# Kernel optimization log

Hardware: AMD Instinct MI355X
Metric: run time of the kernel (lower is better)

## Reference

```python
import jax, jax.numpy as jnp
import numpy as np

N, E, IN_DIM, D, T, L, B, SLEN, C = 50000, 600000, 128, 128, 4, 2, 2048, 16, 16


def _deg_inv_sqrt(idx, n, dtype):
    deg = jax.ops.segment_sum(jnp.ones(idx.shape, dtype=dtype), idx, num_segments=n)
    return jnp.where(deg > 0, deg ** -0.5, 0.0).astype(dtype)


def gcn_conv(h, edge_index, W, b):
    # PyG GCNConv: add self loops, symmetric norm, x@W, scatter-add, +bias
    n = h.shape[0]
    loop = jnp.arange(n)
    row = jnp.concatenate([edge_index[0], loop])
    col = jnp.concatenate([edge_index[1], loop])
    dis = _deg_inv_sqrt(col, n, h.dtype)
    norm = dis[row] * dis[col]              # [E+N]
    xw = h @ W                               # [N, D]
    msgs = xw[row] * norm[:, None]           # [E+N, D] gather
    out = jax.ops.segment_sum(msgs, col, num_segments=n)
    return out + b


def re_conv(r, edge_index, node_type, W, wtype, b):
    # REConv(norm='both'): left-norm by src out-degree, x@W, type weight,
    # scatter-add to dst, right-norm by dst in-degree, +bias, relu
    n = r.shape[0]
    row, col = edge_index
    dl = _deg_inv_sqrt(row, n, r.dtype)
    x = (r * dl[:, None]) @ W                # [N, T]
    x = x * wtype[node_type][:, None]
    out = jax.ops.segment_sum(x[row], col, num_segments=n)
    dr = _deg_inv_sqrt(col, n, r.dtype)
    out = out * dr[:, None] + b
    return jax.nn.relu(out)


def setup_inputs() -> dict:
    key = jax.random.key(0)
    ks = jax.random.split(key, 10)
    x = jax.random.normal(ks[0], (N, IN_DIM), dtype=jnp.float32)
    label = jax.random.randint(ks[1], (N,), 0, C)
    seqs = jax.random.randint(ks[2], (B, SLEN), 0, N)
    edge_index = jax.random.randint(ks[3], (2, E), 0, N)
    node_type = jnp.sort(jax.random.randint(ks[4], (N,), 0, T))
    s_in = 1.0 / np.sqrt(IN_DIM)
    s_d = 1.0 / np.sqrt(D)
    fcW = jax.random.normal(ks[5], (T, IN_DIM, D), dtype=jnp.float32) * s_in
    fcB = jnp.zeros((T, D), dtype=jnp.float32)
    gcnW = jax.random.normal(ks[6], (L, D, D), dtype=jnp.float32) * s_d
    gcnB = jnp.zeros((L, D), dtype=jnp.float32)
    reW = jax.random.normal(ks[7], (L, T, T), dtype=jnp.float32) * 0.5
    re_wtype = jnp.ones((L, T), dtype=jnp.float32)
    reB = jnp.zeros((L, T), dtype=jnp.float32)
    predW = jax.random.normal(ks[8], (D, C), dtype=jnp.float32) * s_d
    predB = jnp.zeros((C,), dtype=jnp.float32)
    return {"x": x, "label": label, "seqs": seqs, "edge_index": edge_index,
            "node_type": node_type, "fcW": fcW, "fcB": fcB, "gcnW": gcnW,
            "gcnB": gcnB, "reW": reW, "re_wtype": re_wtype, "reB": reB,
            "predW": predW, "predB": predB}


def reference(x, label, seqs, edge_index, node_type, fcW, fcB, gcnW, gcnB,
              reW, re_wtype, reB, predW, predB):
    n = x.shape[0]
    # per-type input projection; node_type is sorted so this equals
    # torch.cat([fc[t](x[node_type==t]) for t])
    h_all = jnp.einsum('ni,tio->tno', x, fcW) + fcB[:, None, :]  # [T, N, D]
    gh = h_all[node_type, jnp.arange(n)]                          # [N, D]
    r = jnp.eye(fcW.shape[0], dtype=x.dtype)[node_type]           # [N, T]
    for l in range(gcnW.shape[0]):
        gh = jax.nn.relu(gcn_conv(gh, edge_index, gcnW[l], gcnB[l]))
        r = re_conv(r, edge_index, node_type, reW[l], re_wtype[l], reB[l])
    ego = seqs[:, 0]
    output = gh[ego] @ predW + predB                               # [B, C]
    return output, label[ego]
```

## Files before the change

### kernel.cpp

```cpp
#include <hip/hip_runtime.h>
#include <hip/hip_bf16.h>


typedef __attribute__((ext_vector_type(8))) short short8;
typedef __attribute__((ext_vector_type(4))) float f32x4;
typedef unsigned short u16;

__device__ __forceinline__ float bf2f(u16 u) {
  union { float f; unsigned int i; } v; v.i = (unsigned int)u << 16; return v.f;
}
__device__ __forceinline__ u16 f2bf(float f) {
  union { float f; unsigned int i; } v; v.f = f;
  return (u16)((v.i + 0x7FFF + ((v.i >> 16) & 1)) >> 16);
}

#define NPB 64

__global__ void k_wt(const float* __restrict__ fcW, const float* __restrict__ gcnW,
                     u16* __restrict__ wt, int T, int total) {
  int i = blockIdx.x * 256 + threadIdx.x;
  if (i >= total) return;
  int m = i >> 14;
  int dk = i & 16383;
  int d = dk >> 7, k = dk & 127;
  const float* src = (m < T) ? (fcW + ((size_t)m << 14)) : (gcnW + ((size_t)(m - T) << 14));
  wt[i] = f2bf(src[k * 128 + d]);
}

#define SWZ(row, byte) ((byte) ^ (((row) & 15) << 4))

__device__ __forceinline__ void stage_wt(char* smem_wt, const u16* __restrict__ wtg,
                                         int t) {
  int row = t >> 1;
  int h = (t & 1) * 64;
  const u16* src = wtg + row * 128 + h;
#pragma unroll
  for (int j = 0; j < 8; ++j) {
    short8 v = *(const short8*)(src + j * 8);
    int byte = row * 256 + (h + j * 8) * 2;
    *(short8*)(smem_wt + SWZ(row, byte)) = v;
  }
}

__device__ __forceinline__ void mfma_core(const char* smem_xs, const char* smem_wt,
                                          int t, f32x4 acc[4][2]) {
  const int lane = t & 63, w = t >> 6;
  const int lr = lane & 15, lk = lane >> 4;
#pragma unroll
  for (int ks = 0; ks < 4; ++ks) {
    const int kb = ks * 64 + lk * 16;
    short8 a[4], b[2];
#pragma unroll
    for (int rg = 0; rg < 4; ++rg) {
      int row = rg * 16 + lr;
      a[rg] = *(const short8*)(smem_xs + SWZ(row, row * 256 + kb));
    }
#pragma unroll
    for (int ch = 0; ch < 2; ++ch) {
      int row = w * 32 + ch * 16 + lr;
      b[ch] = *(const short8*)(smem_wt + SWZ(row, row * 256 + kb));
    }
#pragma unroll
    for (int rg = 0; rg < 4; ++rg)
#pragma unroll
      for (int ch = 0; ch < 2; ++ch)
        acc[rg][ch] = __builtin_amdgcn_mfma_f32_16x16x32_bf16(a[rg], b[ch], acc[rg][ch], 0, 0, 0);
  }
}

__global__ __launch_bounds__(256) void k_fc(const float* __restrict__ x,
                                            const int* __restrict__ node_type,
                                            const u16* __restrict__ wt_fc,
                                            const float* __restrict__ fcB,
                                            u16* __restrict__ gh, int n_nodes) {
  __shared__ char smem[49152];
  char* smem_xs = smem;
  char* smem_wt = smem + 16384;
  const int t = threadIdx.x;
  const int nbase = blockIdx.x * NPB;
  const int nend = min(nbase + NPB, n_nodes);
  const int t0 = node_type[nbase];
  const int t1 = node_type[nend - 1];

  {
    int row = t >> 2;
    int c0 = (t & 3) * 32;
    int node = nbase + row;
    float xv[32];
    if (node < n_nodes) {
      const float4* src = (const float4*)(x + (size_t)node * 128 + c0);
#pragma unroll
      for (int j = 0; j < 8; ++j) ((float4*)xv)[j] = src[j];
    } else {
#pragma unroll
      for (int j = 0; j < 32; ++j) xv[j] = 0.0f;
    }
#pragma unroll
    for (int j = 0; j < 4; ++j) {
      u16 tmp[8];
#pragma unroll
      for (int q = 0; q < 8; ++q) tmp[q] = f2bf(xv[j * 8 + q]);
      int byte = row * 256 + (c0 + j * 8) * 2;
      *(short8*)(smem_xs + SWZ(row, byte)) = *(short8*)tmp;
    }
  }

  const int lane = t & 63, w = t >> 6;
  const int lr = lane & 15, lk = lane >> 4;

  for (int tt = t0; tt <= t1; ++tt) {
    if (tt > t0) __syncthreads();
    stage_wt(smem_wt, wt_fc + ((size_t)tt << 14), t);
    __syncthreads();

    f32x4 acc[4][2];
#pragma unroll
    for (int rg = 0; rg < 4; ++rg)
#pragma unroll
      for (int ch = 0; ch < 2; ++ch) acc[rg][ch] = (f32x4){0.f, 0.f, 0.f, 0.f};
    mfma_core(smem_xs, smem_wt, t, acc);

#pragma unroll
    for (int rg = 0; rg < 4; ++rg) {
#pragma unroll
      for (int reg = 0; reg < 4; ++reg) {
        int node = nbase + rg * 16 + lk * 4 + reg;
        if (node < n_nodes && node_type[node] == tt) {
#pragma unroll
          for (int ch = 0; ch < 2; ++ch) {
            int dout = w * 32 + ch * 16 + lr;
            gh[(size_t)node * 128 + dout] = f2bf(acc[rg][ch][reg] + fcB[tt * 128 + dout]);
          }
        }
      }
    }
  }
}

__global__ __launch_bounds__(256) void k_gemm_scale(const u16* __restrict__ ghin,
                                                    const u16* __restrict__ wtg,
                                                    const float* __restrict__ dis,
                                                    u16* __restrict__ xws, int n_nodes) {
  __shared__ char smem[49152];
  char* smem_xs = smem;
  char* smem_wt = smem + 16384;
  const int t = threadIdx.x;
  const int nbase = blockIdx.x * NPB;

  {
    int row = t >> 2;
    int c0 = (t & 3) * 32;
    int node = nbase + row;
    if (node < n_nodes) {
      const u16* src = ghin + (size_t)node * 128 + c0;
#pragma unroll
      for (int j = 0; j < 4; ++j) {
        short8 v = *(const short8*)(src + j * 8);
        int byte = row * 256 + (c0 + j * 8) * 2;
        *(short8*)(smem_xs + SWZ(row, byte)) = v;
      }
    } else {
      short8 z = (short8){0, 0, 0, 0, 0, 0, 0, 0};
#pragma unroll
      for (int j = 0; j < 4; ++j) {
        int byte = row * 256 + (c0 + j * 8) * 2;
        *(short8*)(smem_xs + SWZ(row, byte)) = z;
      }
    }
  }
  stage_wt(smem_wt, wtg, t);
  __syncthreads();

  f32x4 acc[4][2];
#pragma unroll
  for (int rg = 0; rg < 4; ++rg)
#pragma unroll
    for (int ch = 0; ch < 2; ++ch) acc[rg][ch] = (f32x4){0.f, 0.f, 0.f, 0.f};
  mfma_core(smem_xs, smem_wt, t, acc);

  const int lane = t & 63, w = t >> 6;
  const int lr = lane & 15, lk = lane >> 4;
#pragma unroll
  for (int rg = 0; rg < 4; ++rg) {
#pragma unroll
    for (int reg = 0; reg < 4; ++reg) {
      int node = nbase + rg * 16 + lk * 4 + reg;
      if (node < n_nodes) {
        float s = dis[node];
#pragma unroll
        for (int ch = 0; ch < 2; ++ch) {
          int dout = w * 32 + ch * 16 + lr;
          xws[(size_t)node * 128 + dout] = f2bf(acc[rg][ch][reg] * s);
        }
      }
    }
  }
}

__global__ void k_zero(int* __restrict__ p, int n) {
  int i = blockIdx.x * 256 + threadIdx.x;
  if (i < n) p[i] = 0;
}

__global__ void k_count(const int* __restrict__ col, int* __restrict__ ecnt, int e) {
  int i = blockIdx.x * 256 + threadIdx.x;
  if (i < e) atomicAdd(&ecnt[col[i]], 1);
}

__global__ __launch_bounds__(256) void k_scan1(const int* __restrict__ ecnt,
                                               int* __restrict__ scanex,
                                               int* __restrict__ partials, int n) {
  __shared__ int s[256];
  const int t = threadIdx.x;
  const int i = blockIdx.x * 256 + t;
  int v = (i < n) ? ecnt[i] : 0;
  s[t] = v;
  __syncthreads();
  for (int off = 1; off < 256; off <<= 1) {
    int add = (t >= off) ? s[t - off] : 0;
    __syncthreads();
    s[t] += add;
    __syncthreads();
  }
  if (i < n) scanex[i] = s[t] - v;
  if (t == 255) partials[blockIdx.x] = s[t];
}

__global__ __launch_bounds__(256) void k_scan2(int* __restrict__ partials, int np) {
  __shared__ int s[256];
  const int t = threadIdx.x;
  int v = (t < np) ? partials[t] : 0;
  s[t] = v;
  __syncthreads();
  for (int off = 1; off < 256; off <<= 1) {
    int add = (t >= off) ? s[t - off] : 0;
    __syncthreads();
    s[t] += add;
    __syncthreads();
  }
  if (t < np) partials[t] = s[t] - v;
}

__global__ void k_scan3(const int* __restrict__ scanex, const int* __restrict__ partials,
                        const int* __restrict__ ecnt, int* __restrict__ col_ptr,
                        int* __restrict__ cursor, float* __restrict__ dis,
                        int n, int e_total) {
  int i = blockIdx.x * 256 + threadIdx.x;
  if (i < n) {
    int p = scanex[i] + partials[i >> 8];
    col_ptr[i] = p;
    cursor[i] = p;
    dis[i] = rsqrtf((float)(ecnt[i] + 1));
  }
  if (i == 0) col_ptr[n] = e_total;
}

__global__ void k_fill(const int* __restrict__ row, const int* __restrict__ col,
                       int* __restrict__ cursor, int* __restrict__ edge_row, int e) {
  int i = blockIdx.x * 256 + threadIdx.x;
  if (i < e) {
    int c = col[i];
    int pos = atomicAdd(&cursor[c], 1);
    edge_row[pos] = row[i];
  }
}

__global__ __launch_bounds__(256) void k_gather(const int* __restrict__ col_ptr,
                                                const int* __restrict__ edge_row,
                                                const u16* __restrict__ xws,
                                                const float* __restrict__ dis,
                                                const float* __restrict__ bias,
                                                u16* __restrict__ gh, int n_nodes) {
  const int t = threadIdx.x;
  const int node = blockIdx.x * 4 + (t >> 6);
  if (node >= n_nodes) return;
  const int lane = t & 63;
  const int g = lane & 15;
  const int s = lane >> 4;
  float acc[8] = {0.f, 0.f, 0.f, 0.f, 0.f, 0.f, 0.f, 0.f};
  if (s == 0) {
    short8 v = *(const short8*)(xws + (size_t)node * 128 + g * 8);
#pragma unroll
    for (int j = 0; j < 8; ++j) acc[j] = bf2f((u16)v[j]);
  }
  const int e0 = col_ptr[node], e1 = col_ptr[node + 1];
  for (int e = e0 + s; e < e1; e += 4) {
    int r = edge_row[e];
    short8 v = *(const short8*)(xws + (size_t)r * 128 + g * 8);
#pragma unroll
    for (int j = 0; j < 8; ++j) acc[j] += bf2f((u16)v[j]);
  }
#pragma unroll
  for (int j = 0; j < 8; ++j) {
    acc[j] += __shfl_xor(acc[j], 16);
    acc[j] += __shfl_xor(acc[j], 32);
  }
  if (s == 0) {
    float ds = dis[node];
    u16 o[8];
#pragma unroll
    for (int j = 0; j < 8; ++j)
      o[j] = f2bf(fmaxf(acc[j] * ds + bias[g * 8 + j], 0.f));
    *(short8*)(gh + (size_t)node * 128 + g * 8) = *(short8*)o;
  }
}

__global__ void k_pred(const u16* __restrict__ gh, const int* __restrict__ seqs,
                       const int* __restrict__ label, const float* __restrict__ predW,
                       const float* __restrict__ predB, float* __restrict__ out,
                       float* __restrict__ out_label, int b_total, int n_classes,
                       int slen) {
  int tid = blockIdx.x * 256 + threadIdx.x;
  int b = tid / n_classes;
  if (b >= b_total) return;
  int c = tid - b * n_classes;
  int ego = seqs[(size_t)b * slen];
  const u16* g = gh + (size_t)ego * 128;
  float s = predB[c];
#pragma unroll 8
  for (int i = 0; i < 128; ++i) s += bf2f(g[i]) * predW[i * n_classes + c];
  out[(size_t)b * n_classes + c] = s;
  if (c == 0) out_label[b] = (float)label[ego];
}

extern "C" void kernel_launch(void* const* d_in, const int* in_sizes, int n_in,
                              void* d_out, int out_size, void* d_ws, size_t ws_size,
                              hipStream_t stream) {
  const float* x     = (const float*)d_in[0];
  const int*   label = (const int*)d_in[1];
  const int*   seqs  = (const int*)d_in[2];
  const int*   edge  = (const int*)d_in[3];
  const int*   ntype = (const int*)d_in[4];
  const float* fcW   = (const float*)d_in[5];
  const float* fcB   = (const float*)d_in[6];
  const float* gcnW  = (const float*)d_in[7];
  const float* gcnB  = (const float*)d_in[8];
  const float* predW = (const float*)d_in[12];
  const float* predB = (const float*)d_in[13];

  const int n = in_sizes[0] / 128;
  const int e = in_sizes[3] / 2;
  const int T = in_sizes[5] / (128 * 128);
  const int L = in_sizes[8] / 128;
  const int C = in_sizes[13];
  const int slen = 16;
  const int b_total = in_sizes[2] / slen;

  const int* row = edge;
  const int* col = edge + e;

  char* ws = (char*)d_ws;
  const size_t node_bf = (size_t)n * 128 * sizeof(u16);
  u16*   gh      = (u16*)ws;                 ws += node_bf;
  u16*   xws     = (u16*)ws;                 ws += node_bf;
  u16*   wt      = (u16*)ws;                 ws += (size_t)(T + L) * 16384 * 2;
  float* dis     = (float*)ws;               ws += (size_t)n * 4;
  int*   ecnt    = (int*)ws;                 ws += (size_t)n * 4;
  int*   scanex  = (int*)ws;                 ws += (size_t)n * 4;
  int*   col_ptr = (int*)ws;                 ws += (size_t)(n + 16) * 4;
  int*   cursor  = (int*)ws;                 ws += (size_t)n * 4;
  int*   partial = (int*)ws;                 ws += 1024 * 4;
  int*   edge_row= (int*)ws;                 ws += (size_t)e * 4;

  float* out_logits = (float*)d_out;
  float* out_label  = out_logits + (size_t)b_total * C;

  const int nb = (n + NPB - 1) / NPB;
  const int nscan = (n + 255) / 256;
  const int wt_total = (T + L) * 16384;

  hipLaunchKernelGGL(k_wt, dim3((wt_total + 255) / 256), dim3(256), 0, stream,
                     fcW, gcnW, wt, T, wt_total);
  hipLaunchKernelGGL(k_fc, dim3(nb), dim3(256), 0, stream, x, ntype, wt, fcB, gh, n);

  hipLaunchKernelGGL(k_zero, dim3(nscan), dim3(256), 0, stream, ecnt, n);
  hipLaunchKernelGGL(k_count, dim3((e + 255) / 256), dim3(256), 0, stream, col, ecnt, e);
  hipLaunchKernelGGL(k_scan1, dim3(nscan), dim3(256), 0, stream, ecnt, scanex, partial, n);
  hipLaunchKernelGGL(k_scan2, dim3(1), dim3(256), 0, stream, partial, nscan);
  hipLaunchKernelGGL(k_scan3, dim3(nscan), dim3(256), 0, stream, scanex, partial, ecnt,
                     col_ptr, cursor, dis, n, e);
  hipLaunchKernelGGL(k_fill, dim3((e + 255) / 256), dim3(256), 0, stream, row, col,
                     cursor, edge_row, e);

  for (int l = 0; l < L; ++l) {
    hipLaunchKernelGGL(k_gemm_scale, dim3(nb), dim3(256), 0, stream,
                       gh, wt + (size_t)(T + l) * 16384, dis, xws, n);
    hipLaunchKernelGGL(k_gather, dim3((n + 3) / 4), dim3(256), 0, stream,
                       col_ptr, edge_row, xws, dis, gcnB + (size_t)l * 128, gh, n);
  }
  hipLaunchKernelGGL(k_pred, dim3((b_total * C + 255) / 256), dim3(256), 0, stream,
                     gh, seqs, label, predW, predB, out_logits, out_label,
                     b_total, C, slen);
}
```

Measured before the change: 283.1 us.

## Gather only ego nodes in final GCN layer and widen GEMM tiles to 128 rows

The last GCN layer's aggregation now runs only for the B ego nodes that the prediction head reads, writing into a compact buffer, instead of aggregating all N nodes. This removes most of the final full-graph gather. Separately, the fc and GCN GEMM kernels now process 128 nodes per block with 64KB of LDS and hold the B fragments in registers across k-steps. The larger tile raises register and LDS use and halves the block count, which may lower occupancy.

```diff
diff --git a/kernel.cpp b/kernel.cpp
--- a/kernel.cpp
+++ b/kernel.cpp
@@ -14,7 +14,7 @@
   return (u16)((v.i + 0x7FFF + ((v.i >> 16) & 1)) >> 16);
 }
 
-#define NPB 64
+#define NPB 128
 
 __global__ void k_wt(const float* __restrict__ fcW, const float* __restrict__ gcnW,
                      u16* __restrict__ wt, int T, int total) {
@@ -29,42 +29,55 @@
 
 #define SWZ(row, byte) ((byte) ^ (((row) & 15) << 4))
 
-__device__ __forceinline__ void stage_wt(char* smem_wt, const u16* __restrict__ wtg,
-                                         int t) {
+__device__ __forceinline__ void stage_tile_bf16(char* smem, const u16* __restrict__ gsrc,
+                                                int rows_valid, int t) {
   int row = t >> 1;
   int h = (t & 1) * 64;
-  const u16* src = wtg + row * 128 + h;
-#pragma unroll
-  for (int j = 0; j < 8; ++j) {
-    short8 v = *(const short8*)(src + j * 8);
-    int byte = row * 256 + (h + j * 8) * 2;
-    *(short8*)(smem_wt + SWZ(row, byte)) = v;
-  }
-}
-
-__device__ __forceinline__ void mfma_core(const char* smem_xs, const char* smem_wt,
-                                          int t, f32x4 acc[4][2]) {
+  int byte0 = row * 256 + h * 2;
+  if (row < rows_valid) {
+    const u16* src = gsrc + (size_t)row * 128 + h;
+#pragma unroll
+    for (int j = 0; j < 8; ++j) {
+      short8 v = *(const short8*)(src + j * 8);
+      *(short8*)(smem + SWZ(row, byte0 + j * 16)) = v;
+    }
+  } else {
+    short8 z = (short8){0, 0, 0, 0, 0, 0, 0, 0};
+#pragma unroll
+    for (int j = 0; j < 8; ++j)
+      *(short8*)(smem + SWZ(row, byte0 + j * 16)) = z;
+  }
+}
+
+__device__ __forceinline__ void mfma_core128(const char* xs, const char* wt, int t,
+                                             f32x4 acc[8][2]) {
   const int lane = t & 63, w = t >> 6;
   const int lr = lane & 15, lk = lane >> 4;
+  short8 bfrag[4][2];
 #pragma unroll
   for (int ks = 0; ks < 4; ++ks) {
-    const int kb = ks * 64 + lk * 16;
-    short8 a[4], b[2];
-#pragma unroll
-    for (int rg = 0; rg < 4; ++rg) {
-      int row = rg * 16 + lr;
-      a[rg] = *(const short8*)(smem_xs + SWZ(row, row * 256 + kb));
-    }
+    int kb = ks * 64 + lk * 16;
 #pragma unroll
     for (int ch = 0; ch < 2; ++ch) {
       int row = w * 32 + ch * 16 + lr;
-      b[ch] = *(const short8*)(smem_wt + SWZ(row, row * 256 + kb));
-    }
-#pragma unroll
-    for (int rg = 0; rg < 4; ++rg)
+      bfrag[ks][ch] = *(const short8*)(wt + SWZ(row, row * 256 + kb));
+    }
+  }
+#pragma unroll
+  for (int ks = 0; ks < 4; ++ks) {
+    int kb = ks * 64 + lk * 16;
+    short8 a[8];
+#pragma unroll
+    for (int rg = 0; rg < 8; ++rg) {
+      int row = rg * 16 + lr;
+      a[rg] = *(const short8*)(xs + SWZ(row, row * 256 + kb));
+    }
+#pragma unroll
+    for (int rg = 0; rg < 8; ++rg)
 #pragma unroll
       for (int ch = 0; ch < 2; ++ch)
-        acc[rg][ch] = __builtin_amdgcn_mfma_f32_16x16x32_bf16(a[rg], b[ch], acc[rg][ch], 0, 0, 0);
+        acc[rg][ch] = __builtin_amdgcn_mfma_f32_16x16x32_bf16(a[rg], bfrag[ks][ch],
+                                                              acc[rg][ch], 0, 0, 0);
   }
 }
 
@@ -73,9 +86,9 @@
                                             const u16* __restrict__ wt_fc,
                                             const float* __restrict__ fcB,
                                             u16* __restrict__ gh, int n_nodes) {
-  __shared__ char smem[49152];
+  __shared__ char smem[65536];
   char* smem_xs = smem;
-  char* smem_wt = smem + 16384;
+  char* smem_wt = smem + 32768;
   const int t = threadIdx.x;
   const int nbase = blockIdx.x * NPB;
   const int nend = min(nbase + NPB, n_nodes);
@@ -83,25 +96,24 @@
   const int t1 = node_type[nend - 1];
 
   {
-    int row = t >> 2;
-    int c0 = (t & 3) * 32;
+    int row = t >> 1;
+    int h = (t & 1) * 64;
     int node = nbase + row;
-    float xv[32];
+    int byte0 = row * 256 + h * 2;
     if (node < n_nodes) {
-      const float4* src = (const float4*)(x + (size_t)node * 128 + c0);
-#pragma unroll
-      for (int j = 0; j < 8; ++j) ((float4*)xv)[j] = src[j];
+      const float4* src = (const float4*)(x + (size_t)node * 128 + h);
+#pragma unroll
+      for (int j = 0; j < 8; ++j) {
+        float4 a4 = src[j * 2], b4 = src[j * 2 + 1];
+        u16 tmp[8] = {f2bf(a4.x), f2bf(a4.y), f2bf(a4.z), f2bf(a4.w),
+                      f2bf(b4.x), f2bf(b4.y), f2bf(b4.z), f2bf(b4.w)};
+        *(short8*)(smem_xs + SWZ(row, byte0 + j * 16)) = *(short8*)tmp;
+      }
     } else {
-#pragma unroll
-      for (int j = 0; j < 32; ++j) xv[j] = 0.0f;
-    }
-#pragma unroll
-    for (int j = 0; j < 4; ++j) {
-      u16 tmp[8];
-#pragma unroll
-      for (int q = 0; q < 8; ++q) tmp[q] = f2bf(xv[j * 8 + q]);
-      int byte = row * 256 + (c0 + j * 8) * 2;
-      *(short8*)(smem_xs + SWZ(row, byte)) = *(short8*)tmp;
+      short8 z = (short8){0, 0, 0, 0, 0, 0, 0, 0};
+#pragma unroll
+      for (int j = 0; j < 8; ++j)
+        *(short8*)(smem_xs + SWZ(row, byte0 + j * 16)) = z;
     }
   }
 
@@ -110,27 +122,26 @@
 
   for (int tt = t0; tt <= t1; ++tt) {
     if (tt > t0) __syncthreads();
-    stage_wt(smem_wt, wt_fc + ((size_t)tt << 14), t);
+    stage_tile_bf16(smem_wt, wt_fc + ((size_t)tt << 14), 128, t);
     __syncthreads();
 
-    f32x4 acc[4][2];
-#pragma unroll
-    for (int rg = 0; rg < 4; ++rg)
+    f32x4 acc[8][2];
+#pragma unroll
+    for (int rg = 0; rg < 8; ++rg)
 #pragma unroll
       for (int ch = 0; ch < 2; ++ch) acc[rg][ch] = (f32x4){0.f, 0.f, 0.f, 0.f};
-    mfma_core(smem_xs, smem_wt, t, acc);
-
-#pragma unroll
-    for (int rg = 0; rg < 4; ++rg) {
+    mfma_core128(smem_xs, smem_wt, t, acc);
+
+    float bv0 = fcB[tt * 128 + w * 32 + lr];
+    float bv1 = fcB[tt * 128 + w * 32 + 16 + lr];
+#pragma unroll
+    for (int rg = 0; rg < 8; ++rg) {
 #pragma unroll
       for (int reg = 0; reg < 4; ++reg) {
         int node = nbase + rg * 16 + lk * 4 + reg;
         if (node < n_nodes && node_type[node] == tt) {
-#pragma unroll
-          for (int ch = 0; ch < 2; ++ch) {
-            int dout = w * 32 + ch * 16 + lr;
-            gh[(size_t)node * 128 + dout] = f2bf(acc[rg][ch][reg] + fcB[tt * 128 + dout]);
-          }
+          gh[(size_t)node * 128 + w * 32 + lr]      = f2bf(acc[rg][0][reg] + bv0);
+          gh[(size_t)node * 128 + w * 32 + 16 + lr] = f2bf(acc[rg][1][reg] + bv1);
         }
       }
     }
@@ -141,57 +152,35 @@
                                                     const u16* __restrict__ wtg,
                                                     const float* __restrict__ dis,
                                                     u16* __restrict__ xws, int n_nodes) {
-  __shared__ char smem[49152];
+  __shared__ char smem[65536];
   char* smem_xs = smem;
-  char* smem_wt = smem + 16384;
+  char* smem_wt = smem + 32768;
   const int t = threadIdx.x;
   const int nbase = blockIdx.x * NPB;
 
-  {
-    int row = t >> 2;
-    int c0 = (t & 3) * 32;
-    int node = nbase + row;
-    if (node < n_nodes) {
-      const u16* src = ghin + (size_t)node * 128 + c0;
-#pragma unroll
-      for (int j = 0; j < 4; ++j) {
-        short8 v = *(const short8*)(src + j * 8);
-        int byte = row * 256 + (c0 + j * 8) * 2;
-        *(short8*)(smem_xs + SWZ(row, byte)) = v;
-      }
-    } else {
-      short8 z = (short8){0, 0, 0, 0, 0, 0, 0, 0};
-#pragma unroll
-      for (int j = 0; j < 4; ++j) {
-        int byte = row * 256 + (c0 + j * 8) * 2;
-        *(short8*)(smem_xs + SWZ(row, byte)) = z;
-      }
-    }
-  }
-  stage_wt(smem_wt, wtg, t);
+  stage_tile_bf16(smem_xs, ghin + (size_t)nbase * 128,
+                  min(n_nodes - nbase, NPB), t);
+  stage_tile_bf16(smem_wt, wtg, 128, t);
   __syncthreads();
 
-  f32x4 acc[4][2];
-#pragma unroll
-  for (int rg = 0; rg < 4; ++rg)
+  f32x4 acc[8][2];
+#pragma unroll
+  for (int rg = 0; rg < 8; ++rg)
 #pragma unroll
     for (int ch = 0; ch < 2; ++ch) acc[rg][ch] = (f32x4){0.f, 0.f, 0.f, 0.f};
-  mfma_core(smem_xs, smem_wt, t, acc);
+  mfma_core128(smem_xs, smem_wt, t, acc);
 
   const int lane = t & 63, w = t >> 6;
   const int lr = lane & 15, lk = lane >> 4;
 #pragma unroll
-  for (int rg = 0; rg < 4; ++rg) {
+  for (int rg = 0; rg < 8; ++rg) {
 #pragma unroll
     for (int reg = 0; reg < 4; ++reg) {
       int node = nbase + rg * 16 + lk * 4 + reg;
       if (node < n_nodes) {
         float s = dis[node];
-#pragma unroll
-        for (int ch = 0; ch < 2; ++ch) {
-          int dout = w * 32 + ch * 16 + lr;
-          xws[(size_t)node * 128 + dout] = f2bf(acc[rg][ch][reg] * s);
-        }
+        xws[(size_t)node * 128 + w * 32 + lr]      = f2bf(acc[rg][0][reg] * s);
+        xws[(size_t)node * 128 + w * 32 + 16 + lr] = f2bf(acc[rg][1][reg] * s);
       }
     }
   }
@@ -265,6 +254,42 @@
   }
 }
 
+__device__ __forceinline__ void gather_node(int node, const int* __restrict__ col_ptr,
+                                            const int* __restrict__ edge_row,
+                                            const u16* __restrict__ xws,
+                                            const float* __restrict__ dis,
+                                            const float* __restrict__ bias,
+                                            u16* __restrict__ dst, int lane) {
+  const int g = lane & 15;
+  const int s = lane >> 4;
+  float acc[8] = {0.f, 0.f, 0.f, 0.f, 0.f, 0.f, 0.f, 0.f};
+  if (s == 0) {
+    short8 v = *(const short8*)(xws + (size_t)node * 128 + g * 8);
+#pragma unroll
+    for (int j = 0; j < 8; ++j) acc[j] = bf2f((u16)v[j]);
+  }
+  const int e0 = col_ptr[node], e1 = col_ptr[node + 1];
+  for (int e = e0 + s; e < e1; e += 4) {
+    int r = edge_row[e];
+    short8 v = *(const short8*)(xws + (size_t)r * 128 + g * 8);
+#pragma unroll
+    for (int j = 0; j < 8; ++j) acc[j] += bf2f((u16)v[j]);
+  }
+#pragma unroll
+  for (int j = 0; j < 8; ++j) {
+    acc[j] += __shfl_xor(acc[j], 16);
+    acc[j] += __shfl_xor(acc[j], 32);
+  }
+  if (s == 0) {
+    float ds = dis[node];
+    u16 o[8];
+#pragma unroll
+    for (int j = 0; j < 8; ++j)
+      o[j] = f2bf(fmaxf(acc[j] * ds + bias[g * 8 + j], 0.f));
+    *(short8*)(dst + g * 8) = *(short8*)o;
+  }
+}
+
 __global__ __launch_bounds__(256) void k_gather(const int* __restrict__ col_ptr,
                                                 const int* __restrict__ edge_row,
                                                 const u16* __restrict__ xws,
@@ -274,38 +299,27 @@
   const int t = threadIdx.x;
   const int node = blockIdx.x * 4 + (t >> 6);
   if (node >= n_nodes) return;
-  const int lane = t & 63;
-  const int g = lane & 15;
-  const int s = lane >> 4;
-  float acc[8] = {0.f, 0.f, 0.f, 0.f, 0.f, 0.f, 0.f, 0.f};
-  if (s == 0) {
-    short8 v = *(const short8*)(xws + (size_t)node * 128 + g * 8);
-#pragma unroll
-    for (int j = 0; j < 8; ++j) acc[j] = bf2f((u16)v[j]);
-  }
-  const int e0 = col_ptr[node], e1 = col_ptr[node + 1];
-  for (int e = e0 + s; e < e1; e += 4) {
-    int r = edge_row[e];
-    short8 v = *(const short8*)(xws + (size_t)r * 128 + g * 8);
-#pragma unroll
-    for (int j = 0; j < 8; ++j) acc[j] += bf2f((u16)v[j]);
-  }
-#pragma unroll
-  for (int j = 0; j < 8; ++j) {
-    acc[j] += __shfl_xor(acc[j], 16);
-    acc[j] += __shfl_xor(acc[j], 32);
-  }
-  if (s == 0) {
-    float ds = dis[node];
-    u16 o[8];
-#pragma unroll
-    for (int j = 0; j < 8; ++j)
-      o[j] = f2bf(fmaxf(acc[j] * ds + bias[g * 8 + j], 0.f));
-    *(short8*)(gh + (size_t)node * 128 + g * 8) = *(short8*)o;
-  }
-}
-
-__global__ void k_pred(const u16* __restrict__ gh, const int* __restrict__ seqs,
+  gather_node(node, col_ptr, edge_row, xws, dis, bias,
+              gh + (size_t)node * 128, t & 63);
+}
+
+__global__ __launch_bounds__(256) void k_gather_ego(const int* __restrict__ col_ptr,
+                                                    const int* __restrict__ edge_row,
+                                                    const u16* __restrict__ xws,
+                                                    const float* __restrict__ dis,
+                                                    const float* __restrict__ bias,
+                                                    const int* __restrict__ seqs,
+                                                    u16* __restrict__ gh2,
+                                                    int b_total, int slen) {
+  const int t = threadIdx.x;
+  const int b = blockIdx.x * 4 + (t >> 6);
+  if (b >= b_total) return;
+  int node = seqs[(size_t)b * slen];
+  gather_node(node, col_ptr, edge_row, xws, dis, bias,
+              gh2 + (size_t)b * 128, t & 63);
+}
+
+__global__ void k_pred(const u16* __restrict__ gh2, const int* __restrict__ seqs,
                        const int* __restrict__ label, const float* __restrict__ predW,
                        const float* __restrict__ predB, float* __restrict__ out,
                        float* __restrict__ out_label, int b_total, int n_classes,
@@ -314,13 +328,12 @@
   int b = tid / n_classes;
   if (b >= b_total) return;
   int c = tid - b * n_classes;
-  int ego = seqs[(size_t)b * slen];
-  const u16* g = gh + (size_t)ego * 128;
+  const u16* g = gh2 + (size_t)b * 128;
   float s = predB[c];
 #pragma unroll 8
   for (int i = 0; i < 128; ++i) s += bf2f(g[i]) * predW[i * n_classes + c];
   out[(size_t)b * n_classes + c] = s;
-  if (c == 0) out_label[b] = (float)label[ego];
+  if (c == 0) out_label[b] = (float)label[seqs[(size_t)b * slen]];
 }
 
 extern "C" void kernel_launch(void* const* d_in, const int* in_sizes, int n_in,
@@ -353,6 +366,7 @@
   const size_t node_bf = (size_t)n * 128 * sizeof(u16);
   u16*   gh      = (u16*)ws;                 ws += node_bf;
   u16*   xws     = (u16*)ws;                 ws += node_bf;
+  u16*   gh2     = (u16*)ws;                 ws += (size_t)b_total * 128 * 2;
   u16*   wt      = (u16*)ws;                 ws += (size_t)(T + L) * 16384 * 2;
   float* dis     = (float*)ws;               ws += (size_t)n * 4;
   int*   ecnt    = (int*)ws;                 ws += (size_t)n * 4;
@@ -385,10 +399,16 @@
   for (int l = 0; l < L; ++l) {
     hipLaunchKernelGGL(k_gemm_scale, dim3(nb), dim3(256), 0, stream,
                        gh, wt + (size_t)(T + l) * 16384, dis, xws, n);
-    hipLaunchKernelGGL(k_gather, dim3((n + 3) / 4), dim3(256), 0, stream,
-                       col_ptr, edge_row, xws, dis, gcnB + (size_t)l * 128, gh, n);
+    if (l < L - 1) {
+      hipLaunchKernelGGL(k_gather, dim3((n + 3) / 4), dim3(256), 0, stream,
+                         col_ptr, edge_row, xws, dis, gcnB + (size_t)l * 128, gh, n);
+    } else {
+      hipLaunchKernelGGL(k_gather_ego, dim3((b_total + 3) / 4), dim3(256), 0, stream,
+                         col_ptr, edge_row, xws, dis, gcnB + (size_t)l * 128,
+                         seqs, gh2, b_total, slen);
+    }
   }
   hipLaunchKernelGGL(k_pred, dim3((b_total * C + 255) / 256), dim3(256), 0, stream,
-                     gh, seqs, label, predW, predB, out_logits, out_label,
+                     gh2, seqs, label, predW, predB, out_logits, out_label,
                      b_total, C, slen);
 }
```

Measured after the change: 259.9 us. 1.09x faster.
